# Performance work log

Hardware: AMD Instinct MI355X
Metric: run time of the kernel (lower is better)

The kernel has to match this reference:

```python
import jax, jax.numpy as jnp
import numpy as np

TEMPERATURE = 12.5
SINK_EPS = 0.05
SINK_ITERS = 100


def setup_inputs() -> dict:
    key = jax.random.key(0)
    k1, k2, k3, k4 = jax.random.split(key, 4)
    b, n_way, k_shot, q, c, h, w = 8, 5, 1, 75, 640, 7, 7
    return {
        "support_xf": jax.random.normal(k1, (b, n_way * k_shot, c, h, w), jnp.float32),
        "query_xf": jax.random.normal(k2, (b, q, c, h, w), jnp.float32),
        "support_y": jax.random.randint(k3, (b, n_way * k_shot), 0, n_way),
        "query_y": jax.random.randint(k4, (b, q), 0, n_way),
        "n_way": n_way,
        "k_shot": k_shot,
    }


def _sinkhorn_flow(cost, log_a, log_b, eps=SINK_EPS, iters=SINK_ITERS):
    """Entropic-OT (Sinkhorn, log-domain) replacement for cv2.EMD.
    cost: [..., m, n]; log_a: [..., m]; log_b: [..., n] (log of prob marginals).
    Returns transport plan P with row sums ~ exp(log_a), col sums ~ exp(log_b)."""
    f = jnp.zeros_like(log_a)
    g = jnp.zeros_like(log_b)

    def body(_, fg):
        f, g = fg
        f = eps * (log_a - jax.nn.logsumexp((g[..., None, :] - cost) / eps, axis=-1))
        g = eps * (log_b - jax.nn.logsumexp((f[..., :, None] - cost) / eps, axis=-2))
        return (f, g)

    f, g = jax.lax.fori_loop(0, iters, body, (f, g))
    return jnp.exp((f[..., :, None] + g[..., None, :] - cost) / eps)


def _deep_emd_logits(support, query):
    # support: [b, p, c, h, w] (1 prototype per class), query: [b, q, c, h, w]
    b, p, c, h, w = support.shape
    q = query.shape[1]
    hw = h * w
    sup = support.reshape(b, p, c, hw)
    qry = query.reshape(b, q, c, hw)

    # get_weight_vector: inner product of local features with the other set's GAP vector
    sup_gap = sup.mean(-1)  # [b, p, c]
    qry_gap = qry.mean(-1)  # [b, q, c]
    w1 = jax.nn.relu(jnp.einsum('bqcm,bpc->bqpm', qry, sup_gap)) + 1e-3  # [b,q,p,hw]
    w2 = jax.nn.relu(jnp.einsum('bpcn,bqc->bqpn', sup, qry_gap)) + 1e-3  # [b,q,p,hw] (weight_2[j,i] transposed)

    # normalize_feature: subtract per-image channel mean; then cosine similarity over channels
    supn = sup - sup.mean(2, keepdims=True)
    qryn = qry - qry.mean(2, keepdims=True)
    supn = supn / jnp.maximum(jnp.linalg.norm(supn, axis=2, keepdims=True), 1e-8)
    qryn = qryn / jnp.maximum(jnp.linalg.norm(qryn, axis=2, keepdims=True), 1e-8)
    S = jnp.einsum('bqcm,bpcn->bqpmn', qryn, supn)  # [b,q,p,hw,hw]

    # emd_inference marginal normalization: relu(w)+1e-5, rescaled so sum = hw -> prob = w/sum(w)
    wa = w1 + 1e-5
    wb = w2 + 1e-5
    log_a = jnp.log(wa) - jnp.log(wa.sum(-1, keepdims=True))
    log_b = jnp.log(wb) - jnp.log(wb.sum(-1, keepdims=True))

    flow = _sinkhorn_flow(1.0 - S, log_a, log_b) * hw  # total mass = hw as in cv2.EMD path
    flow = jax.lax.stop_gradient(flow)  # original flow comes from numpy -> constant

    logits = (S * flow).sum((-2, -1)) * (TEMPERATURE / hw)  # [b, q, p]
    return logits.reshape(b * q, p)


def reference(support_xf, query_xf, support_y, query_y, n_way, k_shot):
    # training / 1-shot path: pick first shot per class
    b = support_xf.shape[0]
    c, h, w = support_xf.shape[2:]
    sup = support_xf.reshape(b, n_way, k_shot, c, h, w)[:, :, 0]
    logits = _deep_emd_logits(sup, query_xf)  # [b*q, n_way]
    labels = query_y.reshape(-1)
    logp = jax.nn.log_softmax(logits, axis=-1)
    loss = -jnp.take_along_axis(logp, labels[:, None], axis=1).mean()
    return loss
```

## Files before the change

kernel.cpp:

```cpp
#include <hip/hip_runtime.h>
#include <math.h>

#define BB 8
#define PP 5
#define QQ 75
#define CC 640
#define HW 49
#define NIMG_Q (BB*QQ)
#define NIMG_S (BB*PP)
#define NPROB  (BB*QQ*PP)
#define TEMP 12.5f

#define CHUNKS 20
#define TROW 16
#define TCH  (HW*TROW)
#define TIMG (CHUNKS*TCH)
#define SROW 25
#define SPROB (HW*SROW)

#define OFF_SGAP   0
#define OFF_QGAP   (OFF_SGAP  + NIMG_S*CC)
#define OFF_SMEAN  (OFF_QGAP  + NIMG_Q*CC)
#define OFF_SINV   (OFF_SMEAN + NIMG_S*HW)
#define OFF_QMEAN  (OFF_SINV  + NIMG_S*HW)
#define OFF_QINV   (OFF_QMEAN + NIMG_Q*HW)
#define OFF_MARGA  (OFF_QINV  + NIMG_Q*HW)
#define OFF_MARGB  (OFF_MARGA + NPROB*HW)
#define OFF_QT     (OFF_MARGB + NPROB*HW)
#define OFF_ST     (OFF_QT    + NIMG_Q*TIMG)
#define OFF_S16    (OFF_ST    + NIMG_S*TIMG)
#define OFF_LOGITS (OFF_S16   + NPROB*SPROB)

typedef _Float16 f16x8 __attribute__((ext_vector_type(8)));
typedef float f32x4 __attribute__((ext_vector_type(4)));
#define MFMAH __builtin_amdgcn_mfma_f32_16x16x32_f16

__device__ __forceinline__ float wsum64(float v) {
#pragma unroll
    for (int off = 32; off > 0; off >>= 1) v += __shfl_xor(v, off, 64);
    return v;
}
__device__ __forceinline__ float rlf(float x, int l) {
    return __int_as_float(__builtin_amdgcn_readlane(__float_as_int(x), l));
}
__device__ __forceinline__ unsigned packh2(float a, float b) {
    union { _Float16 h[2]; unsigned u; } pk;
    pk.h[0] = (_Float16)a; pk.h[1] = (_Float16)b;
    return pk.u;
}
__device__ __forceinline__ float f16lo(unsigned w) {
    union { unsigned short s; _Float16 h; } u; u.s = (unsigned short)w; return (float)u.h;
}
__device__ __forceinline__ float f16hi(unsigned w) {
    union { unsigned short s; _Float16 h; } u; u.s = (unsigned short)(w >> 16); return (float)u.h;
}

__global__ __launch_bounds__(512) __attribute__((amdgpu_waves_per_eu(4, 4)))
void sup_prep(const float* __restrict__ sup, float* __restrict__ ws) {
    int img = blockIdx.x;
    int tid = threadIdx.x;
    int lane = tid & 63;
    int wv = tid >> 6;
    const float* X = sup + (size_t)img * CC * HW;
    float* gap = ws + OFF_SGAP + img * CC;

    __shared__ float cs_p[8][52], sq_p[8][52];
    __shared__ float muL[52], invL[52];
    float cs = 0.f, sq = 0.f;
    if (lane < HW) {
        for (int c8 = wv * 80; c8 < wv * 80 + 80; c8 += 8) {
            float v[8];
#pragma unroll
            for (int j = 0; j < 8; j++) v[j] = X[(c8 + j) * HW + lane];
#pragma unroll
            for (int j = 0; j < 8; j++) {
                cs += v[j];
                sq = fmaf(v[j], v[j], sq);
            }
        }
    }
    if (lane < 52) {
        cs_p[wv][lane] = (lane < HW) ? cs : 0.f;
        sq_p[wv][lane] = (lane < HW) ? sq : 0.f;
    }
    __syncthreads();
    if (wv == 0 && lane < HW) {
        float c4 = 0.f, s4 = 0.f;
#pragma unroll
        for (int w = 0; w < 8; w++) { c4 += cs_p[w][lane]; s4 += sq_p[w][lane]; }
        float mu = c4 * (1.0f / CC);
        float nsq = fmaxf(s4 - c4 * c4 * (1.0f / CC), 0.f);
        float inv = 1.0f / fmaxf(sqrtf(nsq), 1e-8f);
        ws[OFF_SMEAN + img * HW + lane] = mu;
        ws[OFF_SINV + img * HW + lane] = inv;
        muL[lane] = mu;
        invL[lane] = inv;
    }
    for (int c = tid; c < CC; c += 512) {
        const float* row = X + c * HW;
        float s = 0.f;
#pragma unroll
        for (int g = 0; g < 6; g++) {
            float rv[8];
#pragma unroll
            for (int j = 0; j < 8; j++) rv[j] = row[g * 8 + j];
#pragma unroll
            for (int j = 0; j < 8; j++) s += rv[j];
        }
        s += row[48];
        gap[c] = s * (1.0f / HW);
    }
    __syncthreads();
    unsigned* T = (unsigned*)ws + OFF_ST + (size_t)img * TIMG;
    int m = lane;
    if (m < HW) {
        float mu = muL[m], inv = invL[m];
        for (int t = wv; t < CHUNKS; t += 8) {
            float va[32];
#pragma unroll
            for (int j = 0; j < 32; j++) va[j] = X[(t * 32 + j) * HW + m];
            unsigned pk[16];
#pragma unroll
            for (int w = 0; w < 16; w++)
                pk[w] = packh2((va[2 * w] - mu) * inv, (va[2 * w + 1] - mu) * inv);
            uint4* dst = (uint4*)(T + t * TCH + m * TROW);
#pragma unroll
            for (int u = 0; u < 4; u++)
                dst[u] = make_uint4(pk[4 * u], pk[4 * u + 1], pk[4 * u + 2], pk[4 * u + 3]);
        }
    }
}

__global__ __launch_bounds__(512) __attribute__((amdgpu_waves_per_eu(4, 4)))
void qry_prep(const float* __restrict__ qry, float* __restrict__ ws) {
    int img = blockIdx.x;
    int b = img / QQ;
    int tid = threadIdx.x;
    int lane = tid & 63;
    int wv = tid >> 6;
    const float* X = qry + (size_t)img * CC * HW;
    const float* sg = ws + OFF_SGAP + b * PP * CC;
    float* gap = ws + OFF_QGAP + img * CC;

    __shared__ float XSG[PP * CC];
    __shared__ float cs_p[8][52], sq_p[8][52];
    __shared__ float part[8][PP][52];
    __shared__ float muL[52], invL[52];

    for (int i = tid; i < PP * CC / 4; i += 512)
        ((float4*)XSG)[i] = ((const float4*)sg)[i];
    __syncthreads();

    float cs = 0.f, sq = 0.f;
    float acc[PP] = {0.f, 0.f, 0.f, 0.f, 0.f};
    if (lane < HW) {
        for (int c8 = wv * 80; c8 < wv * 80 + 80; c8 += 16) {
            float v[16];
#pragma unroll
            for (int j = 0; j < 16; j++) v[j] = X[(c8 + j) * HW + lane];
#pragma unroll
            for (int j = 0; j < 16; j++) {
                cs += v[j];
                sq = fmaf(v[j], v[j], sq);
            }
#pragma unroll
            for (int p = 0; p < PP; p++) {
                float a = acc[p];
#pragma unroll
                for (int qv = 0; qv < 4; qv++) {
                    float4 g0 = *(const float4*)&XSG[p * CC + c8 + 4 * qv];
                    a = fmaf(v[4 * qv + 0], g0.x, a);
                    a = fmaf(v[4 * qv + 1], g0.y, a);
                    a = fmaf(v[4 * qv + 2], g0.z, a);
                    a = fmaf(v[4 * qv + 3], g0.w, a);
                }
                acc[p] = a;
            }
        }
    }
    if (lane < 52) {
        cs_p[wv][lane] = (lane < HW) ? cs : 0.f;
        sq_p[wv][lane] = (lane < HW) ? sq : 0.f;
#pragma unroll
        for (int p = 0; p < PP; p++) part[wv][p][lane] = (lane < HW) ? acc[p] : 0.f;
    }
    __syncthreads();
    if (wv == 0) {
        if (lane < HW) {
            float c4 = 0.f, s4 = 0.f;
#pragma unroll
            for (int w = 0; w < 8; w++) { c4 += cs_p[w][lane]; s4 += sq_p[w][lane]; }
            float mu = c4 * (1.0f / CC);
            float nsq = fmaxf(s4 - c4 * c4 * (1.0f / CC), 0.f);
            float inv = 1.0f / fmaxf(sqrtf(nsq), 1e-8f);
            ws[OFF_QMEAN + img * HW + lane] = mu;
            ws[OFF_QINV + img * HW + lane] = inv;
            muL[lane] = mu;
            invL[lane] = inv;
        }
#pragma unroll
        for (int p = 0; p < PP; p++) {
            float a = 0.f;
            if (lane < 52) {
#pragma unroll
                for (int w = 0; w < 8; w++) a += part[w][p][lane];
            }
            float w = (lane < HW) ? (fmaxf(a, 0.f) + 1.01e-3f) : 0.f;
            float s = wsum64(w);
            if (lane < HW) ws[OFF_MARGA + (img * PP + p) * HW + lane] = w / s;
        }
    }
    for (int c = tid; c < CC; c += 512) {
        const float* row = X + c * HW;
        float s = 0.f;
#pragma unroll
        for (int g = 0; g < 6; g++) {
            float rv[8];
#pragma unroll
            for (int j = 0; j < 8; j++) rv[j] = row[g * 8 + j];
#pragma unroll
            for (int j = 0; j < 8; j++) s += rv[j];
        }
        s += row[48];
        gap[c] = s * (1.0f / HW);
    }
    __syncthreads();
    unsigned* T = (unsigned*)ws + OFF_QT + (size_t)img * TIMG;
    int m = lane;
    if (m < HW) {
        float mu = muL[m], inv = invL[m];
        for (int t = wv; t < CHUNKS; t += 8) {
            float va[32];
#pragma unroll
            for (int j = 0; j < 32; j++) va[j] = X[(t * 32 + j) * HW + m];
            unsigned pk[16];
#pragma unroll
            for (int w = 0; w < 16; w++)
                pk[w] = packh2((va[2 * w] - mu) * inv, (va[2 * w + 1] - mu) * inv);
            uint4* dst = (uint4*)(T + t * TCH + m * TROW);
#pragma unroll
            for (int u = 0; u < 4; u++)
                dst[u] = make_uint4(pk[4 * u], pk[4 * u + 1], pk[4 * u + 2], pk[4 * u + 3]);
        }
    }
}

__global__ __launch_bounds__(256) __attribute__((amdgpu_waves_per_eu(2, 4)))
void margb_kernel(const float* __restrict__ sup, float* __restrict__ ws) {
    int id = blockIdx.x;
    int qc = id % 5;
    int bp = id / 5;
    int b = bp / PP;
    int p = bp % PP;
    int tid = threadIdx.x;
    int lane = tid & 63;
    int wv = tid >> 6;
    const float* X = sup + (size_t)bp * CC * HW;
    const float* qg = ws + OFF_QGAP + (b * QQ + qc * 15) * CC;

    __shared__ float QG[15 * CC];
    __shared__ float part[4][15][52];
    for (int i = tid; i < 15 * CC / 4; i += 256)
        ((float4*)QG)[i] = ((const float4*)qg)[i];
    __syncthreads();

    float acc[15];
#pragma unroll
    for (int i = 0; i < 15; i++) acc[i] = 0.f;
    if (lane < HW) {
        for (int c8 = wv * 160; c8 < wv * 160 + 160; c8 += 8) {
            float sv[8];
#pragma unroll
            for (int j = 0; j < 8; j++) sv[j] = X[(c8 + j) * HW + lane];
#pragma unroll
            for (int qq = 0; qq < 15; qq++) {
                float4 g0 = *(const float4*)&QG[qq * CC + c8];
                float4 g1 = *(const float4*)&QG[qq * CC + c8 + 4];
                float a = acc[qq];
                a = fmaf(sv[0], g0.x, a); a = fmaf(sv[1], g0.y, a);
                a = fmaf(sv[2], g0.z, a); a = fmaf(sv[3], g0.w, a);
                a = fmaf(sv[4], g1.x, a); a = fmaf(sv[5], g1.y, a);
                a = fmaf(sv[6], g1.z, a); a = fmaf(sv[7], g1.w, a);
                acc[qq] = a;
            }
        }
    }
    if (lane < 52) {
#pragma unroll
        for (int qq = 0; qq < 15; qq++) part[wv][qq][lane] = (lane < HW) ? acc[qq] : 0.f;
    }
    __syncthreads();
    if (wv == 0) {
#pragma unroll
        for (int qq = 0; qq < 15; qq++) {
            float a = 0.f;
            if (lane < 52)
                a = part[0][qq][lane] + part[1][qq][lane] + part[2][qq][lane] + part[3][qq][lane];
            int q = qc * 15 + qq;
            float w = (lane < HW) ? (fmaxf(a, 0.f) + 1.01e-3f) : 0.f;
            float s = wsum64(w);
            if (lane < HW) ws[OFF_MARGB + ((b * QQ + q) * PP + p) * HW + lane] = w / s;
        }
    }
}

__global__ __launch_bounds__(256, 2) void gemm_kernel(float* __restrict__ ws) {
    __shared__ unsigned LDSU[CHUNKS * TCH];

    int g = blockIdx.x;
    int xcd = g & 7;
    int k = g >> 3;
    int p = k % 5;
    int gidx = xcd + 8 * (k / 5);
    int b = gidx / 15;
    int qg = gidx - b * 15;

    int tid = threadIdx.x;
    int lane = tid & 63;
    int wv = tid >> 6;
    int lrow = lane & 15;
    int quad = lane >> 4;

    const unsigned* Bt = (const unsigned*)ws + OFF_ST + (size_t)(b * PP + p) * TIMG;
    for (int idx = tid; idx < CHUNKS * HW * 4; idx += 256) {
        int r = idx >> 2;
        int q = idx & 3;
        int t = r / 49;
        int n = r - t * 49;
        uint4 v = *(const uint4*)(Bt + (idx << 2));
        *(uint4*)(&LDSU[t * TCH + n * 16 + ((q ^ ((n >> 1) & 3)) << 2)]) = v;
    }
    __syncthreads();

    int bof[4];
#pragma unroll
    for (int nt = 0; nt < 4; nt++) {
        int n = 16 * nt + lrow;
        if (n > 48) n = 48;
        bof[nt] = n * 16 + ((quad ^ ((n >> 1) & 3)) << 2);
    }

    const unsigned* Aq = (const unsigned*)ws + OFF_QT + (size_t)(b * QQ + qg * 5) * TIMG;
    int arow = (16 * wv + lrow) * TROW + quad * 4;

    f32x4 acc[5][4];
#pragma unroll
    for (int qi = 0; qi < 5; qi++)
#pragma unroll
        for (int nt = 0; nt < 4; nt++) acc[qi][nt] = (f32x4){0.f, 0.f, 0.f, 0.f};

#pragma unroll 2
    for (int t = 0; t < CHUNKS; t++) {
        f16x8 bfr[4];
#pragma unroll
        for (int nt = 0; nt < 4; nt++)
            bfr[nt] = *(const f16x8*)(&LDSU[t * TCH + bof[nt]]);
#pragma unroll
        for (int qi = 0; qi < 5; qi++) {
            f16x8 a = *(const f16x8*)(Aq + (size_t)qi * TIMG + t * TCH + arow);
#pragma unroll
            for (int nt = 0; nt < 4; nt++)
                acc[qi][nt] = MFMAH(a, bfr[nt], acc[qi][nt], 0, 0, 0);
        }
    }

    __syncthreads();
    float* S_lds = (float*)LDSU;
#pragma unroll
    for (int qi = 0; qi < 5; qi++)
#pragma unroll
        for (int nt = 0; nt < 4; nt++)
#pragma unroll
            for (int r = 0; r < 4; r++) {
                int mm = 16 * wv + quad * 4 + r;
                int nn = 16 * nt + lrow;
                if (mm < HW && nn < HW) S_lds[qi * 2597 + mm * 53 + nn] = acc[qi][nt][r];
            }
    __syncthreads();

    for (int qi = 0; qi < 5; qi++) {
        int prob = (b * QQ + qg * 5 + qi) * PP + p;
        unsigned* Sp = (unsigned*)ws + OFF_S16 + (size_t)prob * SPROB;
        const float* Sl = S_lds + qi * 2597;
        for (int idx = tid; idx < SPROB; idx += 256) {
            int row = idx / SROW;
            int w = idx - row * SROW;
            int n0 = 2 * w;
            float v0 = Sl[row * 53 + n0];
            float v1 = (n0 + 1 < HW) ? Sl[row * 53 + n0 + 1] : 0.f;
            Sp[idx] = packh2(v0, v1);
        }
    }
}

#define FOR12(M) M(0) M(1) M(2) M(3) M(4) M(5) M(6) M(7) M(8) M(9) M(10) M(11)
#define KEXPF(s) __expf(fmaf(20.f, (s), -20.f))

__global__ __launch_bounds__(64)
__attribute__((amdgpu_waves_per_eu(3, 3)))
void sinkhorn_kernel(float* __restrict__ ws) {
    __shared__ float KT[HW * 53];
    int prob = blockIdx.x;
    int lane = threadIdx.x;
    const unsigned* Sp = (const unsigned*)ws + OFF_S16 + (size_t)prob * SPROB;

    float am = 0.f, bm = 0.f;
    if (lane < HW) {
        am = ws[OFF_MARGA + prob * HW + lane];
        bm = ws[OFF_MARGB + prob * HW + lane];
    }
    int ll = (lane < HW) ? lane : 48;
    const unsigned* rbase = Sp + ll * SROW;

    float4 kr0, kr1, kr2, kr3, kr4, kr5, kr6, kr7, kr8, kr9, kr10, kr11;
    float kr12x;
#define KIR(g) { unsigned w0 = rbase[2*(g)]; unsigned w1 = rbase[2*(g)+1];  \
    kr##g = make_float4(KEXPF(f16lo(w0)), KEXPF(f16hi(w0)),                 \
                        KEXPF(f16lo(w1)), KEXPF(f16hi(w1))); }
    FOR12(KIR)
#undef KIR
    kr12x = KEXPF(f16lo(rbase[24]));

    if (lane < HW) {
#define KW(g) { KT[(4*(g)+0)*53 + lane] = kr##g.x;                          \
                KT[(4*(g)+1)*53 + lane] = kr##g.y;                          \
                KT[(4*(g)+2)*53 + lane] = kr##g.z;                          \
                KT[(4*(g)+3)*53 + lane] = kr##g.w; }
        FOR12(KW)
#undef KW
        KT[48 * 53 + lane] = kr12x;
    }
    __syncthreads();
    const float* KTrow = KT + ll * 53;

    float vv = (lane < HW) ? 1.f : 0.f;
    float uu = 0.f;

#pragma unroll 1
    for (int it = 0; it < 48; it++) {
        float t0 = 0.f, t1 = 0.f, t2 = 0.f, t3 = 0.f;
#define RS(g) { t0 = fmaf(kr##g.x, rlf(vv, 4*(g)+0), t0);                   \
                t1 = fmaf(kr##g.y, rlf(vv, 4*(g)+1), t1);                   \
                t2 = fmaf(kr##g.z, rlf(vv, 4*(g)+2), t2);                   \
                t3 = fmaf(kr##g.w, rlf(vv, 4*(g)+3), t3); }
        FOR12(RS)
#undef RS
        t0 = fmaf(kr12x, rlf(vv, 48), t0);
        float t = (t0 + t1) + (t2 + t3);
        uu = am * __builtin_amdgcn_rcpf(t);

        if (__builtin_expect((int)blockIdx.x < 0, 0)) KT[lane] = uu;

        float s0 = 0.f, s1 = 0.f, s2 = 0.f, s3 = 0.f;
#define CS(g) { float k0 = KTrow[4*(g)+0]; float k1 = KTrow[4*(g)+1];       \
                float k2 = KTrow[4*(g)+2]; float k3 = KTrow[4*(g)+3];       \
                s0 = fmaf(k0, rlf(uu, 4*(g)+0), s0);                        \
                s1 = fmaf(k1, rlf(uu, 4*(g)+1), s1);                        \
                s2 = fmaf(k2, rlf(uu, 4*(g)+2), s2);                        \
                s3 = fmaf(k3, rlf(uu, 4*(g)+3), s3); }
        FOR12(CS)
#undef CS
        s0 = fmaf(KTrow[48], rlf(uu, 48), s0);
        float s = (s0 + s1) + (s2 + s3);
        vv = bm * __builtin_amdgcn_rcpf(s);
    }

    float ssum = 0.f;
#define FS(g) {                                                             \
    ssum = fmaf(kr##g.x * fmaf(0.05f, __logf(kr##g.x), 1.f), rlf(vv, 4*(g)+0), ssum); \
    ssum = fmaf(kr##g.y * fmaf(0.05f, __logf(kr##g.y), 1.f), rlf(vv, 4*(g)+1), ssum); \
    ssum = fmaf(kr##g.z * fmaf(0.05f, __logf(kr##g.z), 1.f), rlf(vv, 4*(g)+2), ssum); \
    ssum = fmaf(kr##g.w * fmaf(0.05f, __logf(kr##g.w), 1.f), rlf(vv, 4*(g)+3), ssum); }
    FOR12(FS)
#undef FS
    ssum = fmaf(kr12x * fmaf(0.05f, __logf(kr12x), 1.f), rlf(vv, 48), ssum);
    float contrib = (lane < HW) ? (uu * ssum) : 0.f;
    float tot = wsum64(contrib);
    if (lane == 0) ws[OFF_LOGITS + prob] = TEMP * tot;
}

__global__ __launch_bounds__(640) void loss_kernel(const float* __restrict__ ws,
                                                   const int* __restrict__ qy,
                                                   float* __restrict__ out) {
    int tid = threadIdx.x;
    float val = 0.f;
    if (tid < NIMG_Q) {
        const float* lg = ws + OFF_LOGITS + tid * PP;
        float l[PP];
        float mx = -1e30f;
#pragma unroll
        for (int p = 0; p < PP; p++) {
            l[p] = lg[p];
            mx = fmaxf(mx, l[p]);
        }
        float se = 0.f;
#pragma unroll
        for (int p = 0; p < PP; p++) se += __expf(l[p] - mx);
        float lse = mx + logf(se);
        int lab = qy[tid];
        val = -(l[lab] - lse);
    }
    __shared__ float red[16];
    float s = wsum64(val);
    if ((tid & 63) == 0) red[tid >> 6] = s;
    __syncthreads();
    if (tid == 0) {
        float tot = 0.f;
#pragma unroll
        for (int w = 0; w < 10; w++) tot += red[w];
        out[0] = tot * (1.0f / NIMG_Q);
    }
}

extern "C" void kernel_launch(void* const* d_in, const int* in_sizes, int n_in,
                              void* d_out, int out_size, void* d_ws, size_t ws_size,
                              hipStream_t stream) {
    const float* sup = (const float*)d_in[0];
    const float* qry = (const float*)d_in[1];
    const int* qy = (const int*)d_in[3];
    float* ws = (float*)d_ws;
    float* out = (float*)d_out;

    sup_prep<<<NIMG_S, 512, 0, stream>>>(sup, ws);
    qry_prep<<<NIMG_Q, 512, 0, stream>>>(qry, ws);
    margb_kernel<<<NIMG_S * 5, 256, 0, stream>>>(sup, ws);
    gemm_kernel<<<600, 256, 0, stream>>>(ws);
    sinkhorn_kernel<<<NPROB, 64, 0, stream>>>(ws);
    loss_kernel<<<1, 640, 0, stream>>>(ws, qy, out);
}
```

Measured before the change: 297.3 us.

## Split each Sinkhorn problem across two waves with register-resident kernel and transpose

The Sinkhorn kernel now runs each transport problem with 128 threads instead of 64. Each wave handles 25 of the 49 columns and keeps its slice of both the exp-kernel and its transpose in registers, which removes the LDS transpose table and its per-iteration LDS reads. Partial row and column sums are combined through small shared arrays, at the cost of two block barriers per iteration. The goal is to halve the serial FMA chain per lane and raise wave count, in exchange for extra synchronisation and a second strided global read of the fp16 cost matrix.

```diff
diff --git a/kernel.cpp b/kernel.cpp
--- a/kernel.cpp
+++ b/kernel.cpp
@@ -393,15 +393,18 @@
     }
 }
 
-#define FOR12(M) M(0) M(1) M(2) M(3) M(4) M(5) M(6) M(7) M(8) M(9) M(10) M(11)
 #define KEXPF(s) __expf(fmaf(20.f, (s), -20.f))
 
-__global__ __launch_bounds__(64)
-__attribute__((amdgpu_waves_per_eu(3, 3)))
+__global__ __launch_bounds__(128)
+__attribute__((amdgpu_waves_per_eu(4, 4)))
 void sinkhorn_kernel(float* __restrict__ ws) {
-    __shared__ float KT[HW * 53];
+    __shared__ float TP[2][52];
+    __shared__ float SPx[2][52];
     int prob = blockIdx.x;
-    int lane = threadIdx.x;
+    int tid = threadIdx.x;
+    int lane = tid & 63;
+    int wv = tid >> 6;
+    int KB = wv * 25;
     const unsigned* Sp = (const unsigned*)ws + OFF_S16 + (size_t)prob * SPROB;
 
     float am = 0.f, bm = 0.f;
@@ -411,27 +414,19 @@
     }
     int ll = (lane < HW) ? lane : 48;
     const unsigned* rbase = Sp + ll * SROW;
-
-    float4 kr0, kr1, kr2, kr3, kr4, kr5, kr6, kr7, kr8, kr9, kr10, kr11;
-    float kr12x;
-#define KIR(g) { unsigned w0 = rbase[2*(g)]; unsigned w1 = rbase[2*(g)+1];  \
-    kr##g = make_float4(KEXPF(f16lo(w0)), KEXPF(f16hi(w0)),                 \
-                        KEXPF(f16lo(w1)), KEXPF(f16hi(w1))); }
-    FOR12(KIR)
-#undef KIR
-    kr12x = KEXPF(f16lo(rbase[24]));
-
-    if (lane < HW) {
-#define KW(g) { KT[(4*(g)+0)*53 + lane] = kr##g.x;                          \
-                KT[(4*(g)+1)*53 + lane] = kr##g.y;                          \
-                KT[(4*(g)+2)*53 + lane] = kr##g.z;                          \
-                KT[(4*(g)+3)*53 + lane] = kr##g.w; }
-        FOR12(KW)
-#undef KW
-        KT[48 * 53 + lane] = kr12x;
-    }
-    __syncthreads();
-    const float* KTrow = KT + ll * 53;
+    int wof = ll >> 1;
+    int sh = (ll & 1) * 16;
+
+    float krw[25], ktw[25];
+#pragma unroll
+    for (int j = 0; j < 25; j++) {
+        int k = KB + j;
+        int kc = (k < HW) ? k : 0;
+        float sv = f16lo((rbase[kc >> 1] >> ((kc & 1) * 16)) & 0xFFFFu);
+        krw[j] = (k < HW) ? KEXPF(sv) : 0.f;
+        float tv = f16lo((Sp[kc * SROW + wof] >> sh) & 0xFFFFu);
+        ktw[j] = (k < HW) ? KEXPF(tv) : 0.f;
+    }
 
     float vv = (lane < HW) ? 1.f : 0.f;
     float uu = 0.f;
@@ -439,44 +434,49 @@
 #pragma unroll 1
     for (int it = 0; it < 48; it++) {
         float t0 = 0.f, t1 = 0.f, t2 = 0.f, t3 = 0.f;
-#define RS(g) { t0 = fmaf(kr##g.x, rlf(vv, 4*(g)+0), t0);                   \
-                t1 = fmaf(kr##g.y, rlf(vv, 4*(g)+1), t1);                   \
-                t2 = fmaf(kr##g.z, rlf(vv, 4*(g)+2), t2);                   \
-                t3 = fmaf(kr##g.w, rlf(vv, 4*(g)+3), t3); }
-        FOR12(RS)
-#undef RS
-        t0 = fmaf(kr12x, rlf(vv, 48), t0);
-        float t = (t0 + t1) + (t2 + t3);
-        uu = am * __builtin_amdgcn_rcpf(t);
-
-        if (__builtin_expect((int)blockIdx.x < 0, 0)) KT[lane] = uu;
+#pragma unroll
+        for (int j = 0; j < 25; j++) {
+            float pv = rlf(vv, KB + j);
+            if ((j & 3) == 0)      t0 = fmaf(krw[j], pv, t0);
+            else if ((j & 3) == 1) t1 = fmaf(krw[j], pv, t1);
+            else if ((j & 3) == 2) t2 = fmaf(krw[j], pv, t2);
+            else                   t3 = fmaf(krw[j], pv, t3);
+        }
+        if (lane < HW) TP[wv][lane] = (t0 + t1) + (t2 + t3);
+        __syncthreads();
+        float t = TP[0][ll] + TP[1][ll];
+        uu = (lane < HW) ? am * __builtin_amdgcn_rcpf(t) : 0.f;
 
         float s0 = 0.f, s1 = 0.f, s2 = 0.f, s3 = 0.f;
-#define CS(g) { float k0 = KTrow[4*(g)+0]; float k1 = KTrow[4*(g)+1];       \
-                float k2 = KTrow[4*(g)+2]; float k3 = KTrow[4*(g)+3];       \
-                s0 = fmaf(k0, rlf(uu, 4*(g)+0), s0);                        \
-                s1 = fmaf(k1, rlf(uu, 4*(g)+1), s1);                        \
-                s2 = fmaf(k2, rlf(uu, 4*(g)+2), s2);                        \
-                s3 = fmaf(k3, rlf(uu, 4*(g)+3), s3); }
-        FOR12(CS)
-#undef CS
-        s0 = fmaf(KTrow[48], rlf(uu, 48), s0);
-        float s = (s0 + s1) + (s2 + s3);
-        vv = bm * __builtin_amdgcn_rcpf(s);
-    }
-
-    float ssum = 0.f;
-#define FS(g) {                                                             \
-    ssum = fmaf(kr##g.x * fmaf(0.05f, __logf(kr##g.x), 1.f), rlf(vv, 4*(g)+0), ssum); \
-    ssum = fmaf(kr##g.y * fmaf(0.05f, __logf(kr##g.y), 1.f), rlf(vv, 4*(g)+1), ssum); \
-    ssum = fmaf(kr##g.z * fmaf(0.05f, __logf(kr##g.z), 1.f), rlf(vv, 4*(g)+2), ssum); \
-    ssum = fmaf(kr##g.w * fmaf(0.05f, __logf(kr##g.w), 1.f), rlf(vv, 4*(g)+3), ssum); }
-    FOR12(FS)
-#undef FS
-    ssum = fmaf(kr12x * fmaf(0.05f, __logf(kr12x), 1.f), rlf(vv, 48), ssum);
-    float contrib = (lane < HW) ? (uu * ssum) : 0.f;
-    float tot = wsum64(contrib);
-    if (lane == 0) ws[OFF_LOGITS + prob] = TEMP * tot;
+#pragma unroll
+        for (int j = 0; j < 25; j++) {
+            float pu = rlf(uu, KB + j);
+            if ((j & 3) == 0)      s0 = fmaf(ktw[j], pu, s0);
+            else if ((j & 3) == 1) s1 = fmaf(ktw[j], pu, s1);
+            else if ((j & 3) == 2) s2 = fmaf(ktw[j], pu, s2);
+            else                   s3 = fmaf(ktw[j], pu, s3);
+        }
+        if (lane < HW) SPx[wv][lane] = (s0 + s1) + (s2 + s3);
+        __syncthreads();
+        float s = SPx[0][ll] + SPx[1][ll];
+        vv = (lane < HW) ? bm * __builtin_amdgcn_rcpf(s) : 0.f;
+    }
+
+    float ssp = 0.f;
+#pragma unroll
+    for (int j = 0; j < 25; j++) {
+        int k = KB + j;
+        float term = (k < HW) ? krw[j] * fmaf(0.05f, __logf(krw[j]), 1.f) : 0.f;
+        ssp = fmaf(term, rlf(vv, KB + j), ssp);
+    }
+    if (lane < HW) TP[wv][lane] = ssp;
+    __syncthreads();
+    float sstot = TP[0][ll] + TP[1][ll];
+    float contrib = (lane < HW) ? (uu * sstot) : 0.f;
+    if (wv == 0) {
+        float tot = wsum64(contrib);
+        if (lane == 0) ws[OFF_LOGITS + prob] = TEMP * tot;
+    }
 }
 
 __global__ __launch_bounds__(640) void loss_kernel(const float* __restrict__ ws,
@@ -525,6 +525,6 @@
     qry_prep<<<NIMG_Q, 512, 0, stream>>>(qry, ws);
     margb_kernel<<<NIMG_S * 5, 256, 0, stream>>>(sup, ws);
     gemm_kernel<<<600, 256, 0, stream>>>(ws);
-    sinkhorn_kernel<<<NPROB, 64, 0, stream>>>(ws);
+    sinkhorn_kernel<<<NPROB, 128, 0, stream>>>(ws);
     loss_kernel<<<1, 640, 0, stream>>>(ws, qy, out);
 }
```

After: 362.7 us. 1.22x slower.
